# Kernel optimization log

Hardware: AMD Instinct MI355X
Metric: run time of the kernel (lower is better)

The kernel has to match this reference:

```python
import jax, jax.numpy as jnp
import numpy as np

L = 14  # max_relative_position
H = 12  # num_heads
HD = 64  # head_dim


def rel_pos_embed(N, table_v, table_h):
    # 2D relative-position embedding with a leading CLS token (index 0).
    n = N - 1
    s = int(n ** 0.5)  # grid side (14)
    r = jnp.arange(n)
    dv = r[None, :] // s - r[:, None] // s  # vertical distance
    dh = r[None, :] % s - r[:, None] % s   # horizontal distance
    iv = jnp.clip(dv, -L, L) + L + 1
    ih = jnp.clip(dh, -L, L) + L + 1
    iv = jnp.pad(iv, ((1, 0), (1, 0)))  # CLS row/col -> index 0
    ih = jnp.pad(ih, ((1, 0), (1, 0)))
    return table_v[iv] + table_h[ih]  # [N, N, HD]


def setup_inputs() -> dict:
    key = jax.random.key(0)
    ks = jax.random.split(key, 11)
    B, N, E = 64, 197, 768
    T = 2 * L + 2  # rel-pos table rows (30)
    std = 0.02
    return {
        "x": jax.random.normal(ks[0], (B, N, E), jnp.float32),
        "wq": jax.random.normal(ks[1], (E, H * HD), jnp.float32) * std,
        "wk": jax.random.normal(ks[2], (E, H * HD), jnp.float32) * std,
        "wv": jax.random.normal(ks[3], (E, H * HD), jnp.float32) * std,
        "wproj": jax.random.normal(ks[4], (H * HD, E), jnp.float32) * std,
        "bproj": jnp.zeros((E,), jnp.float32),
        "rk_v": jax.random.normal(ks[5], (T, HD), jnp.float32) * std,
        "rk_h": jax.random.normal(ks[6], (T, HD), jnp.float32) * std,
        "rv_v": jax.random.normal(ks[7], (T, HD), jnp.float32) * std,
        "rv_h": jax.random.normal(ks[8], (T, HD), jnp.float32) * std,
    }


def reference(x, wq, wk, wv, wproj, bproj, rk_v, rk_h, rv_v, rv_h):
    B, N, E = x.shape
    scale = HD ** -0.5
    q = (x @ wq).reshape(B, N, H, HD).transpose(0, 2, 1, 3)  # [B,H,N,HD]
    k = (x @ wk).reshape(B, N, H, HD).transpose(0, 2, 1, 3)
    v = (x @ wv).reshape(B, N, H, HD).transpose(0, 2, 1, 3)

    attn = jnp.einsum('bhid,bhjd->bhij', q, k) * scale
    rpk = rel_pos_embed(N, rk_v, rk_h)  # [N,N,HD]
    attn = attn + jnp.einsum('bhid,ijd->bhij', q, rpk) * scale
    attn = jax.nn.softmax(attn, axis=-1)

    out = jnp.einsum('bhij,bhjd->bhid', attn, v)
    rpv = rel_pos_embed(N, rv_v, rv_h)
    out = out + jnp.einsum('bhij,ijd->bhid', attn, rpv)

    out = out.transpose(0, 2, 1, 3).reshape(B, N, H * HD)
    return out @ wproj + bproj
```

## Files before the change

### kernel.cpp

```cpp
#include <hip/hip_runtime.h>
#include <math.h>

typedef _Float16 f16;
typedef __attribute__((ext_vector_type(8))) _Float16 f16x8;
typedef __attribute__((ext_vector_type(4))) _Float16 f16x4;
typedef __attribute__((ext_vector_type(4))) float f32x4;

#define NH 12
#define HDIM 64
#define NTOK 197
#define EDIM 768
#define NB 64
#define MROWS (NB*NTOK)

__global__ __launch_bounds__(256) void convert_x(
    const float* __restrict__ x, f16* __restrict__ xh)
{
    int idx = blockIdx.x * 256 + threadIdx.x;
    const float4* s = (const float4*)x + (size_t)idx * 2;
    float4 a = s[0], b = s[1];
    f16x8 h;
    h[0]=(f16)a.x; h[1]=(f16)a.y; h[2]=(f16)a.z; h[3]=(f16)a.w;
    h[4]=(f16)b.x; h[5]=(f16)b.y; h[6]=(f16)b.z; h[7]=(f16)b.w;
    *(f16x8*)(xh + (size_t)idx * 8) = h;
}

__global__ __launch_bounds__(256) void transpose_w(
    const float* __restrict__ wq, const float* __restrict__ wk,
    const float* __restrict__ wv, const float* __restrict__ wp,
    f16* __restrict__ wqkvT, f16* __restrict__ wpT)
{
    __shared__ float T[64][65];
    int m = blockIdx.z;
    const float* src = (m==0)?wq:(m==1)?wk:(m==2)?wv:wp;
    int k0 = blockIdx.x * 64, n0 = blockIdx.y * 64;
    int cidx = threadIdx.x & 63, r4 = threadIdx.x >> 6;
#pragma unroll
    for (int rr = 0; rr < 16; ++rr) {
        int kl = rr*4 + r4;
        T[kl][cidx] = src[(size_t)(k0+kl)*EDIM + n0 + cidx];
    }
    __syncthreads();
    f16* dst = (m < 3) ? (wqkvT + (size_t)m*EDIM*EDIM) : wpT;
#pragma unroll
    for (int rr = 0; rr < 16; ++rr) {
        int nl = rr*4 + r4;
        dst[(size_t)(n0+nl)*EDIM + k0 + cidx] = (f16)T[cidx][nl];
    }
}

__global__ __launch_bounds__(256) void gemm_h(
    const f16* __restrict__ A, const f16* __restrict__ Bt,
    f16* __restrict__ q_o, f16* __restrict__ k_o, f16* __restrict__ v_o,
    float* __restrict__ p_o, const float* __restrict__ bias, int mode)
{
    __shared__ f16 As[128*64];
    __shared__ f16 Bs[128*64];

    const int tid = threadIdx.x;
    const int l  = tid & 63;
    const int w  = tid >> 6;
    const int lr = l & 15, lq = l >> 4;
    const int wr = w >> 1, wc = w & 1;
    const int m0 = blockIdx.y * 128, n0 = blockIdx.x * 128;

    const int sr = tid >> 3, sc = (tid & 7) << 3;
    const int sw = (sr & 7) << 3;
    const int dsoff = sr * 64 + (sc ^ sw);

    const f16* agp[4]; const f16* bgp[4];
#pragma unroll
    for (int p = 0; p < 4; ++p) {
        int ra = m0 + p*32 + sr; if (ra >= MROWS) ra = MROWS - 1;
        agp[p] = A  + (size_t)ra * EDIM + sc;
        bgp[p] = Bt + (size_t)(n0 + p*32 + sr) * EDIM + sc;
    }

    f16x8 ar_[4], br_[4];
#pragma unroll
    for (int p = 0; p < 4; ++p) {
        ar_[p] = *(const f16x8*)agp[p];
        br_[p] = *(const f16x8*)bgp[p];
    }

    f32x4 acc[4][4];
#pragma unroll
    for (int mt = 0; mt < 4; ++mt)
#pragma unroll
        for (int nt = 0; nt < 4; ++nt) {
            acc[mt][nt][0]=0.f; acc[mt][nt][1]=0.f;
            acc[mt][nt][2]=0.f; acc[mt][nt][3]=0.f;
        }

    for (int kt = 0; kt < 12; ++kt) {
        __syncthreads();
#pragma unroll
        for (int p = 0; p < 4; ++p) {
            *(f16x8*)&As[p*2048 + dsoff] = ar_[p];
            *(f16x8*)&Bs[p*2048 + dsoff] = br_[p];
        }
        if (kt < 11) {
            int ko = (kt + 1) * 64;
#pragma unroll
            for (int p = 0; p < 4; ++p) {
                ar_[p] = *(const f16x8*)(agp[p] + ko);
                br_[p] = *(const f16x8*)(bgp[p] + ko);
            }
        }
        __syncthreads();
#pragma unroll
        for (int ks = 0; ks < 2; ++ks) {
            const int kb = ks*32 + lq*8;
            f16x8 af[4], bf[4];
#pragma unroll
            for (int mt = 0; mt < 4; ++mt) {
                int Ra = wr*64 + mt*16 + lr;
                af[mt] = *(const f16x8*)&As[Ra*64 + (kb ^ ((Ra&7)<<3))];
                int Rb = wc*64 + mt*16 + lr;
                bf[mt] = *(const f16x8*)&Bs[Rb*64 + (kb ^ ((Rb&7)<<3))];
            }
#pragma unroll
            for (int mt = 0; mt < 4; ++mt)
#pragma unroll
                for (int nt = 0; nt < 4; ++nt)
                    acc[mt][nt] = __builtin_amdgcn_mfma_f32_16x16x32_f16(
                        af[mt], bf[nt], acc[mt][nt], 0, 0, 0);
        }
    }

    if (mode == 0) {
        const int mat   = n0 / EDIM;
        const int hbase = ((n0 % EDIM) >> 6) + wc;
        f16* dst = (mat == 0) ? q_o : (mat == 1) ? k_o : v_o;
#pragma unroll
        for (int mt = 0; mt < 4; ++mt)
#pragma unroll
            for (int rg = 0; rg < 4; ++rg) {
                int R = m0 + wr*64 + mt*16 + lq*4 + rg;
                if (R < MROWS) {
                    int bb = R / NTOK, nn = R - bb * NTOK;
                    f16* base = dst + (((size_t)(bb*NH + hbase))*NTOK + nn) * HDIM;
#pragma unroll
                    for (int nt = 0; nt < 4; ++nt)
                        base[nt*16 + lr] = (f16)acc[mt][nt][rg];
                }
            }
    } else {
#pragma unroll
        for (int mt = 0; mt < 4; ++mt)
#pragma unroll
            for (int rg = 0; rg < 4; ++rg) {
                int R = m0 + wr*64 + mt*16 + lq*4 + rg;
                if (R < MROWS) {
                    float* base = p_o + (size_t)R * EDIM + n0 + wc*64;
#pragma unroll
                    for (int nt = 0; nt < 4; ++nt) {
                        int c = nt*16 + lr;
                        base[c] = acc[mt][nt][rg] + bias[n0 + wc*64 + c];
                    }
                }
            }
    }
}

#define SKE 104
#define SVT 320
#define SGT 232
#define SWS 72

__device__ __forceinline__ void wfence() {
    asm volatile("s_waitcnt lgkmcnt(0)" ::: "memory");
    __builtin_amdgcn_sched_barrier(0);
    __builtin_amdgcn_wave_barrier();
}

__device__ __forceinline__ unsigned div14(unsigned n) { return (n * 4682u) >> 16; }

__global__ __launch_bounds__(768, 1) void attn_mfma(
    const f16* __restrict__ q_ws, const f16* __restrict__ k_ws,
    const f16* __restrict__ v_ws,
    const float* __restrict__ rkv, const float* __restrict__ rkh,
    const float* __restrict__ rvv, const float* __restrict__ rvh,
    f16* __restrict__ o_ws)
{
    __shared__ f16 Kle[272*SKE];
    __shared__ f16 Vt[64*SVT];
    __shared__ f16 Gt[32*SGT];
    __shared__ f16 WSh[12*16*SWS];

    const int tid = threadIdx.x;
    const int w = tid >> 6, l = tid & 63;
    const int lr = l & 15, lq = l >> 4;
    const int bh = blockIdx.x;
    const int b = bh / NH, h = bh - b * NH;
    const f16* Qp = q_ws + (size_t)bh * NTOK * HDIM;
    const f16* Kp = k_ws + (size_t)bh * NTOK * HDIM;
    const f16* Vp = v_ws + (size_t)bh * NTOK * HDIM;
    f16* wsh = &WSh[w * 16 * SWS];

    for (int idx = tid; idx < 272*13; idx += 768) {
        int row = idx / 13, c = idx - row*13;
        int c8 = c << 3;
        f16x8 hv;
#pragma unroll
        for (int e = 0; e < 8; ++e) hv[e] = (f16)0.f;
        if (c < 8) {
            if (row < NTOK) {
                hv = *(const f16x8*)(Kp + row*64 + c8);
            } else if (row >= 208 && row < 238) {
                const float* src = rkv + (row-208)*64 + c8;
                float4 a = *(const float4*)src, d = *(const float4*)(src+4);
                hv[0]=(f16)a.x; hv[1]=(f16)a.y; hv[2]=(f16)a.z; hv[3]=(f16)a.w;
                hv[4]=(f16)d.x; hv[5]=(f16)d.y; hv[6]=(f16)d.z; hv[7]=(f16)d.w;
            } else if (row >= 240 && row < 270) {
                const float* src = rkh + (row-240)*64 + c8;
                float4 a = *(const float4*)src, d = *(const float4*)(src+4);
                hv[0]=(f16)a.x; hv[1]=(f16)a.y; hv[2]=(f16)a.z; hv[3]=(f16)a.w;
                hv[4]=(f16)d.x; hv[5]=(f16)d.y; hv[6]=(f16)d.z; hv[7]=(f16)d.w;
            }
        } else if (c < 12 && row < 208) {
            int gbase = (c - 8) << 3;
            if (row == 0) {
#pragma unroll
                for (int e = 0; e < 8; ++e) {
                    int g = gbase + e;
                    hv[e] = (g == 14 || g == 30) ? (f16)1.f : (f16)0.f;
                }
            } else if (row <= 196) {
                int rm = row - 1;
                int gv = (int)div14((unsigned)rm);
                int gh = rm - gv*14;
#pragma unroll
                for (int e = 0; e < 8; ++e) {
                    int g = gbase + e;
                    hv[e] = (g == gv || g == 16 + gh) ? (f16)1.f : (f16)0.f;
                }
            }
        }
        *(f16x8*)&Kle[row*SKE + c8] = hv;
    }

    for (int idx = tid; idx < 8*SVT; idx += 768) {
        int dlow = idx & 7, k = idx >> 3;
        int kx = k ^ (dlow << 3);
        bool isV = (k < NTOK), isA = (k >= 208 && k < 238), isB = (k >= 238 && k < 268);
#pragma unroll
        for (int e = 0; e < 8; ++e) {
            int d = (e << 3) + dlow;
            f16 val = (f16)0.f;
            if (isV)      val = Vp[k*64 + d];
            else if (isA) val = (f16)rvv[(k-208)*64 + d];
            else if (isB) val = (f16)rvh[(k-238)*64 + d];
            Vt[d*SVT + kx] = val;
        }
    }

    for (int idx = tid; idx < 32*29; idx += 768) {
        int g = idx / 29, c = idx - g*29, c8 = c << 3;
        f16x8 hv;
#pragma unroll
        for (int e = 0; e < 8; ++e) hv[e] = (f16)0.f;
        if (g < 14 || (g >= 16 && g < 30)) {
#pragma unroll
            for (int e = 0; e < 8; ++e) {
                int j = c8 + e;
                if (j >= 1 && j <= 196) {
                    int jm = j - 1;
                    int gv = (int)div14((unsigned)jm);
                    int gh = jm - gv*14;
                    if ((g < 14 && gv == g) || (g >= 16 && gh == g - 16))
                        hv[e] = (f16)1.f;
                }
            }
        }
        *(f16x8*)&Gt[g*SGT + c8] = hv;
    }
    __syncthreads();

    const int src0 = ((l >> 4) & 1) * 32 + lr;
    const int src1 = src0 + 16;

    for (int tt = w; tt < 13; tt += 12) {
        const int i0 = tt * 16;
        const int iq = i0 + lr;
        const int iqc = (iq > 196) ? 196 : iq;
        const f16* qsrc = Qp + iqc*64 + lq*8;
        f16x8 qf0 = *(const f16x8*)qsrc;
        f16x8 qf1 = *(const f16x8*)(qsrc + 32);

        __builtin_amdgcn_s_setprio(1);
        f32x4 pacc[4];
#pragma unroll
        for (int ct = 0; ct < 4; ++ct) {
            f32x4 a; a[0]=0.f; a[1]=0.f; a[2]=0.f; a[3]=0.f;
            const int krow = (13+ct)*16 + lr;
            f16x8 kf0 = *(f16x8*)&Kle[krow*SKE + lq*8];
            f16x8 kf1 = *(f16x8*)&Kle[krow*SKE + 32 + lq*8];
            a = __builtin_amdgcn_mfma_f32_16x16x32_f16(kf0, qf0, a, 0, 0, 0);
            a = __builtin_amdgcn_mfma_f32_16x16x32_f16(kf1, qf1, a, 0, 0, 0);
            pacc[ct] = a;
        }
        __builtin_amdgcn_s_setprio(0);
#pragma unroll
        for (int ct = 0; ct < 4; ++ct)
#pragma unroll
            for (int rg = 0; rg < 4; ++rg)
                wsh[lr*SWS + ct*16 + lq*4 + rg] = (f16)pacc[ct][rg];
        wfence();

        int id_ = 0, ih_ = 0;
        const bool qcls = (iq == 0);
        if (iq > 0) { unsigned v = div14((unsigned)(iq-1)); id_ = (int)v; ih_ = (iq-1) - (int)v*14; }
        f16x8 qcf;
#pragma unroll
        for (int e = 0; e < 8; ++e) {
            int g = lq*8 + e;
            int toff;
            if (g < 14)       toff = qcls ? 0 : (g - id_ + 15);
            else if (g == 14) toff = 0;
            else if (g == 15) toff = 63;
            else if (g < 30)  toff = qcls ? 32 : (32 + (g-16) - ih_ + 15);
            else if (g == 30) toff = 32;
            else              toff = 63;
            qcf[e] = wsh[lr*SWS + toff];
        }

        f32x4 acc[13];
        __builtin_amdgcn_s_setprio(1);
#pragma unroll
        for (int ct = 0; ct < 13; ++ct) {
            f32x4 a; a[0]=0.f; a[1]=0.f; a[2]=0.f; a[3]=0.f;
            const int krow = ct*16 + lr;
            f16x8 kf0 = *(f16x8*)&Kle[krow*SKE + lq*8];
            f16x8 kf1 = *(f16x8*)&Kle[krow*SKE + 32 + lq*8];
            f16x8 gf  = *(f16x8*)&Kle[krow*SKE + 64 + lq*8];
            a = __builtin_amdgcn_mfma_f32_16x16x32_f16(kf0, qf0, a, 0, 0, 0);
            a = __builtin_amdgcn_mfma_f32_16x16x32_f16(kf1, qf1, a, 0, 0, 0);
            a = __builtin_amdgcn_mfma_f32_16x16x32_f16(gf,  qcf, a, 0, 0, 0);
            acc[ct] = a;
        }
        __builtin_amdgcn_s_setprio(0);

#pragma unroll
        for (int rg = 0; rg < 4; ++rg)
            if (lq*4 + rg > 4) acc[12][rg] = -1e30f;

        float m = -1e30f;
#pragma unroll
        for (int ct = 0; ct < 13; ++ct)
#pragma unroll
            for (int rg = 0; rg < 4; ++rg) m = fmaxf(m, acc[ct][rg]);
        m = fmaxf(m, __shfl_xor(m, 16));
        m = fmaxf(m, __shfl_xor(m, 32));
        const float C1 = 0.125f * 1.44269504088896f;
        const float nm = -m * C1;
        float ssum = 0.f;
#pragma unroll
        for (int ct = 0; ct < 13; ++ct)
#pragma unroll
            for (int rg = 0; rg < 4; ++rg) {
                float p = exp2f(fmaf(acc[ct][rg], C1, nm));
                acc[ct][rg] = p; ssum += p;
            }
        ssum += __shfl_xor(ssum, 16);
        ssum += __shfl_xor(ssum, 32);
        const float inv = 1.f / ssum;
        const float pn00 = acc[0][0] * inv;

        unsigned pk[13][2];
#pragma unroll
        for (int ct = 0; ct < 13; ++ct) {
            union { f16x4 hh; unsigned u[2]; } t;
            t.hh[0] = (f16)(acc[ct][0] * inv);
            t.hh[1] = (f16)(acc[ct][1] * inv);
            t.hh[2] = (f16)(acc[ct][2] * inv);
            t.hh[3] = (f16)(acc[ct][3] * inv);
            pk[ct][0] = t.u[0]; pk[ct][1] = t.u[1];
        }

        f16x8 pa[7];
#pragma unroll
        for (int kc = 0; kc < 7; ++kc) {
            const int ctA = 2*kc;
            const int ctB = (kc == 6) ? 12 : 2*kc + 1;
            unsigned A0 = (unsigned)__shfl((int)pk[ctA][0], src0);
            unsigned A1 = (unsigned)__shfl((int)pk[ctA][1], src0);
            unsigned A2 = (unsigned)__shfl((int)pk[ctA][0], src1);
            unsigned A3 = (unsigned)__shfl((int)pk[ctA][1], src1);
            unsigned B0 = (unsigned)__shfl((int)pk[ctB][0], src0);
            unsigned B1 = (unsigned)__shfl((int)pk[ctB][1], src0);
            unsigned B2 = (unsigned)__shfl((int)pk[ctB][0], src1);
            unsigned B3 = (unsigned)__shfl((int)pk[ctB][1], src1);
            bool hiHalf = (lq >= 2);
            union { unsigned u[4]; f16x8 v; } f;
            f.u[0] = hiHalf ? B0 : A0;
            f.u[1] = hiHalf ? B1 : A1;
            f.u[2] = hiHalf ? B2 : A2;
            f.u[3] = hiHalf ? B3 : A3;
            if (kc == 6 && hiHalf) { f.u[0]=0; f.u[1]=0; f.u[2]=0; f.u[3]=0; }
            pa[kc] = f.v;
        }

        f32x4 gacc[2];
#pragma unroll
        for (int ct = 0; ct < 2; ++ct) { gacc[ct][0]=0.f; gacc[ct][1]=0.f; gacc[ct][2]=0.f; gacc[ct][3]=0.f; }
        __builtin_amdgcn_s_setprio(1);
#pragma unroll
        for (int kc = 0; kc < 7; ++kc) {
#pragma unroll
            for (int ct = 0; ct < 2; ++ct) {
                f16x8 gf = *(f16x8*)&Gt[(ct*16 + lr)*SGT + kc*32 + lq*8];
                gacc[ct] = __builtin_amdgcn_mfma_f32_16x16x32_f16(pa[kc], gf, gacc[ct], 0, 0, 0);
            }
        }
        __builtin_amdgcn_s_setprio(0);

#pragma unroll
        for (int z = 0; z < 2; ++z) {
            int zi = z*64 + l;
            int zr = zi >> 3, zc = (zi & 7) << 3;
            f16x8 zz;
#pragma unroll
            for (int e = 0; e < 8; ++e) zz[e] = (f16)0.f;
            *(f16x8*)&wsh[zr*SWS + zc] = zz;
        }
        wfence();
#pragma unroll
        for (int rg = 0; rg < 4; ++rg) {
            int il = lq*4 + rg;
            int is_ = i0 + il;
            if (lr < 14 && is_ > 0) {
                unsigned v = div14((unsigned)(is_-1));
                int id2 = (int)v, ih2 = (is_-1) - (int)v*14;
                wsh[il*SWS + (lr - id2 + 15)]      = (f16)gacc[0][rg];
                wsh[il*SWS + 30 + (lr - ih2 + 15)] = (f16)gacc[1][rg];
            }
        }
        if (lq == 0 && !(i0 == 0 && lr == 0)) {
            wsh[lr*SWS + 0]  = (f16)pn00;
            wsh[lr*SWS + 30] = (f16)pn00;
        }
        if (i0 == 0) {
            float sv = (lq == 0) ? gacc[0][0] : 0.f;
            float sh = (lq == 0) ? gacc[1][0] : 0.f;
            sv += __shfl_xor(sv, 1); sv += __shfl_xor(sv, 2);
            sv += __shfl_xor(sv, 4); sv += __shfl_xor(sv, 8);
            sh += __shfl_xor(sh, 1); sh += __shfl_xor(sh, 2);
            sh += __shfl_xor(sh, 4); sh += __shfl_xor(sh, 8);
            if (l == 0) {
                wsh[0]  = (f16)(sv + pn00);
                wsh[30] = (f16)(sh + pn00);
            }
        }
        wfence();

        f16x8 sfr[2];
#pragma unroll
        for (int kc2 = 0; kc2 < 2; ++kc2)
            sfr[kc2] = *(f16x8*)&wsh[lr*SWS + kc2*32 + lq*8];

        f32x4 oacc[4];
#pragma unroll
        for (int ct = 0; ct < 4; ++ct) { oacc[ct][0]=0.f; oacc[ct][1]=0.f; oacc[ct][2]=0.f; oacc[ct][3]=0.f; }
        __builtin_amdgcn_s_setprio(1);
        const int swz = (lr & 7) << 3;
#pragma unroll
        for (int kc = 0; kc < 7; ++kc) {
#pragma unroll
            for (int ct = 0; ct < 4; ++ct) {
                f16x8 vf = *(f16x8*)&Vt[(ct*16 + lr)*SVT + ((kc*32 + lq*8) ^ swz)];
                oacc[ct] = __builtin_amdgcn_mfma_f32_16x16x32_f16(pa[kc], vf, oacc[ct], 0, 0, 0);
            }
        }
#pragma unroll
        for (int kc2 = 0; kc2 < 2; ++kc2) {
#pragma unroll
            for (int ct = 0; ct < 4; ++ct) {
                f16x8 vf = *(f16x8*)&Vt[(ct*16 + lr)*SVT + ((208 + kc2*32 + lq*8) ^ swz)];
                oacc[ct] = __builtin_amdgcn_mfma_f32_16x16x32_f16(sfr[kc2], vf, oacc[ct], 0, 0, 0);
            }
        }
        __builtin_amdgcn_s_setprio(0);

#pragma unroll
        for (int ct = 0; ct < 4; ++ct)
#pragma unroll
            for (int rg = 0; rg < 4; ++rg) {
                int io = i0 + lq*4 + rg;
                if (io < NTOK) {
                    int d = ct*16 + lr;
                    o_ws[((size_t)(b * NTOK + io) * NH + h) * HDIM + d] = (f16)oacc[ct][rg];
                }
            }
    }
}

extern "C" void kernel_launch(void* const* d_in, const int* in_sizes, int n_in,
                              void* d_out, int out_size, void* d_ws, size_t ws_size,
                              hipStream_t stream)
{
    const float* x     = (const float*)d_in[0];
    const float* wq    = (const float*)d_in[1];
    const float* wk    = (const float*)d_in[2];
    const float* wv    = (const float*)d_in[3];
    const float* wproj = (const float*)d_in[4];
    const float* bproj = (const float*)d_in[5];
    const float* rkv   = (const float*)d_in[6];
    const float* rkh   = (const float*)d_in[7];
    const float* rvv   = (const float*)d_in[8];
    const float* rvh   = (const float*)d_in[9];

    f16* ws = (f16*)d_ws;
    const size_t sz = (size_t)MROWS * EDIM;
    f16* xh    = ws;
    f16* qh    = xh + sz;
    f16* kh    = qh + sz;
    f16* vh    = kh + sz;
    f16* oh    = vh + sz;
    f16* wqkvT = oh + sz;
    f16* wpT   = wqkvT + (size_t)3*EDIM*EDIM;

    convert_x  <<<4728, 256, 0, stream>>>(x, xh);
    transpose_w<<<dim3(12, 12, 4), 256, 0, stream>>>(wq, wk, wv, wproj, wqkvT, wpT);
    gemm_h     <<<dim3(18, 99), 256, 0, stream>>>(xh, wqkvT, qh, kh, vh,
                                                  nullptr, nullptr, 0);
    attn_mfma  <<<NB * NH, 768, 0, stream>>>(qh, kh, vh,
                                             rkv, rkh, rvv, rvh, oh);
    gemm_h     <<<dim3(6, 99), 256, 0, stream>>>(oh, wpT, nullptr, nullptr, nullptr,
                                                 (float*)d_out, bproj, 1);
}
```

Before: 177.4 us.

## Use direct global-to-LDS loads and XCD-aware block remapping in GEMM

The GEMM tile loads now use global_load_lds, which writes 16-byte chunks straight into shared memory through a per-lane XOR-swizzled column. This replaces the register-staged prefetch and drops the register round trip. The launch grid becomes 1D, and block ids are remapped so that consecutive tiles land on the same XCD, which should improve L2 reuse. The trade-off is losing the overlap of the next tile's global loads with the current compute, since it is now load, sync, compute, sync with no double buffering.

```diff
diff --git a/kernel.cpp b/kernel.cpp
--- a/kernel.cpp
+++ b/kernel.cpp
@@ -49,10 +49,16 @@
     }
 }
 
+__device__ __forceinline__ void gload16(const f16* g, f16* lds_base) {
+    __builtin_amdgcn_global_load_lds(
+        (const __attribute__((address_space(1))) void*)g,
+        (__attribute__((address_space(3))) void*)lds_base, 16, 0, 0);
+}
+
 __global__ __launch_bounds__(256) void gemm_h(
     const f16* __restrict__ A, const f16* __restrict__ Bt,
     f16* __restrict__ q_o, f16* __restrict__ k_o, f16* __restrict__ v_o,
-    float* __restrict__ p_o, const float* __restrict__ bias, int mode)
+    float* __restrict__ p_o, const float* __restrict__ bias, int mode, int nxb)
 {
     __shared__ f16 As[128*64];
     __shared__ f16 Bs[128*64];
@@ -62,25 +68,26 @@
     const int w  = tid >> 6;
     const int lr = l & 15, lq = l >> 4;
     const int wr = w >> 1, wc = w & 1;
-    const int m0 = blockIdx.y * 128, n0 = blockIdx.x * 128;
-
-    const int sr = tid >> 3, sc = (tid & 7) << 3;
-    const int sw = (sr & 7) << 3;
-    const int dsoff = sr * 64 + (sc ^ sw);
-
-    const f16* agp[4]; const f16* bgp[4];
+
+    const int nwg  = gridDim.x;
+    const int orig = blockIdx.x;
+    const int xcd  = orig & 7;
+    const int qc   = nwg >> 3, rc = nwg & 7;
+    const int wgid = (xcd < rc ? xcd*(qc+1) : rc*(qc+1) + (xcd-rc)*qc) + (orig >> 3);
+    const int mband = wgid / nxb, nband = wgid - mband*nxb;
+    const int m0 = mband << 7, n0 = nband << 7;
+
+    const int scol = (((l & 7) ^ (l >> 3)) << 3);
+    const f16* aG[4]; const f16* bG[4];
+    f16* aL[4]; f16* bL[4];
 #pragma unroll
     for (int p = 0; p < 4; ++p) {
-        int ra = m0 + p*32 + sr; if (ra >= MROWS) ra = MROWS - 1;
-        agp[p] = A  + (size_t)ra * EDIM + sc;
-        bgp[p] = Bt + (size_t)(n0 + p*32 + sr) * EDIM + sc;
-    }
-
-    f16x8 ar_[4], br_[4];
-#pragma unroll
-    for (int p = 0; p < 4; ++p) {
-        ar_[p] = *(const f16x8*)agp[p];
-        br_[p] = *(const f16x8*)bgp[p];
+        int rt = (w*4 + p)*8 + (l >> 3);
+        int ra = m0 + rt; if (ra >= MROWS) ra = MROWS - 1;
+        aG[p] = A  + (size_t)ra * EDIM + scol;
+        bG[p] = Bt + (size_t)(n0 + rt) * EDIM + scol;
+        aL[p] = &As[(w*4 + p) * 512];
+        bL[p] = &Bs[(w*4 + p) * 512];
     }
 
     f32x4 acc[4][4];
@@ -93,19 +100,11 @@
         }
 
     for (int kt = 0; kt < 12; ++kt) {
-        __syncthreads();
+        const int ko = kt * 64;
 #pragma unroll
         for (int p = 0; p < 4; ++p) {
-            *(f16x8*)&As[p*2048 + dsoff] = ar_[p];
-            *(f16x8*)&Bs[p*2048 + dsoff] = br_[p];
-        }
-        if (kt < 11) {
-            int ko = (kt + 1) * 64;
-#pragma unroll
-            for (int p = 0; p < 4; ++p) {
-                ar_[p] = *(const f16x8*)(agp[p] + ko);
-                br_[p] = *(const f16x8*)(bgp[p] + ko);
-            }
+            gload16(aG[p] + ko, aL[p]);
+            gload16(bG[p] + ko, bL[p]);
         }
         __syncthreads();
 #pragma unroll
@@ -126,6 +125,7 @@
                     acc[mt][nt] = __builtin_amdgcn_mfma_f32_16x16x32_f16(
                         af[mt], bf[nt], acc[mt][nt], 0, 0, 0);
         }
+        __syncthreads();
     }
 
     if (mode == 0) {
@@ -522,10 +522,10 @@
 
     convert_x  <<<4728, 256, 0, stream>>>(x, xh);
     transpose_w<<<dim3(12, 12, 4), 256, 0, stream>>>(wq, wk, wv, wproj, wqkvT, wpT);
-    gemm_h     <<<dim3(18, 99), 256, 0, stream>>>(xh, wqkvT, qh, kh, vh,
-                                                  nullptr, nullptr, 0);
+    gemm_h     <<<99*18, 256, 0, stream>>>(xh, wqkvT, qh, kh, vh,
+                                           nullptr, nullptr, 0, 18);
     attn_mfma  <<<NB * NH, 768, 0, stream>>>(qh, kh, vh,
                                              rkv, rkh, rvv, rvh, oh);
-    gemm_h     <<<dim3(6, 99), 256, 0, stream>>>(oh, wpT, nullptr, nullptr, nullptr,
-                                                 (float*)d_out, bproj, 1);
-}
+    gemm_h     <<<99*6, 256, 0, stream>>>(oh, wpT, nullptr, nullptr, nullptr,
+                                          (float*)d_out, bproj, 1, 6);
+}
```

Result: slower. 182.2 us (+2.7%).
